# Optimization experiments

Measured on AMD Instinct MI355X. Metric: run time of the kernel, lower is better.

## Reference

```python
import jax, jax.numpy as jnp
import numpy as np

B, T, HID = 16, 512, 1024
NH, NKV, D = 8, 4, 128
THETA = 10000.0


def setup_inputs() -> dict:
    key = jax.random.key(0)
    k0, k1, k2, k3, k4 = jax.random.split(key, 5)
    s = 0.02
    return {
        "hidden_states": jax.random.normal(k0, (B, T, HID), dtype=jnp.float32),
        "Wq": s * jax.random.normal(k1, (HID, NH * D), dtype=jnp.float32),
        "Wk": s * jax.random.normal(k2, (HID, NKV * D), dtype=jnp.float32),
        "Wv": s * jax.random.normal(k3, (HID, NKV * D), dtype=jnp.float32),
        "Wo": s * jax.random.normal(k4, (NH * D, HID), dtype=jnp.float32),
    }


def _rotate_half(x):
    x1, x2 = x[..., : x.shape[-1] // 2], x[..., x.shape[-1] // 2:]
    return jnp.concatenate((-x2, x1), axis=-1)


def reference(hidden_states, Wq, Wk, Wv, Wo):
    b, t, _ = hidden_states.shape
    # projections -> [B, H, T, D]
    q = (hidden_states @ Wq).reshape(b, t, NH, D).transpose(0, 2, 1, 3)
    k = (hidden_states @ Wk).reshape(b, t, NKV, D).transpose(0, 2, 1, 3)
    v = (hidden_states @ Wv).reshape(b, t, NKV, D).transpose(0, 2, 1, 3)

    # RoPE: cos/sin [T, D]
    inv_freq = 1.0 / (THETA ** (jnp.arange(0, D, 2, dtype=jnp.float32) / D))
    freqs = jnp.outer(jnp.arange(t, dtype=jnp.float32), inv_freq)
    emb = jnp.concatenate((freqs, freqs), axis=-1)
    cos, sin = jnp.cos(emb), jnp.sin(emb)
    q = q * cos + _rotate_half(q) * sin
    k = k * cos + _rotate_half(k) * sin

    # repeat_interleave KV heads to match query heads (GQA)
    groups = NH // NKV
    k = jnp.repeat(k, groups, axis=1)  # [B, NH, T, D]
    v = jnp.repeat(v, groups, axis=1)

    scale = 1.0 / jnp.sqrt(jnp.float32(D))
    attn = jnp.einsum("bhtd,bhsd->bhts", q, k) * scale  # [B, NH, T, T]
    causal = jnp.triu(jnp.ones((t, t), dtype=bool), k=1)
    attn = jnp.where(causal, -jnp.inf, attn)
    attn = jax.nn.softmax(attn, axis=-1)  # dropout p=0 (eval)

    out = jnp.einsum("bhts,bhsd->bhtd", attn, v)
    out = out.transpose(0, 2, 1, 3).reshape(b, t, NH * D)
    return out @ Wo  # [B, T, HID]
```

## Files before the change

### kernel.cpp

```cpp
#include <hip/hip_runtime.h>
#include <hip/hip_bf16.h>
#include <math.h>

#define Bn 16
#define Tn 512
#define HIDn 1024
#define NHn 8
#define NKVn 4
#define Dn 128

typedef __attribute__((ext_vector_type(8))) short short8;
typedef __attribute__((ext_vector_type(4))) float floatx4;

__device__ __forceinline__ short bf16r(float f) {
  __hip_bfloat16 h = __float2bfloat16(f);
  return *(short*)&h;
}
__device__ __forceinline__ float bf16f(short s) {
  __hip_bfloat16 h = *(__hip_bfloat16*)&s;
  return __bfloat162float(h);
}

__device__ __forceinline__ void g2l16(const short* g, short* l) {
  __builtin_amdgcn_global_load_lds(
      (const __attribute__((address_space(1))) void*)g,
      (__attribute__((address_space(3))) void*)l, 16, 0, 0);
}

__global__ __launch_bounds__(256) void prep_kernel(const float* __restrict__ X,
                                                   const float* __restrict__ Wq,
                                                   const float* __restrict__ Wk,
                                                   const float* __restrict__ Wv,
                                                   const float* __restrict__ Wo,
                                                   short* __restrict__ Xb,
                                                   short* __restrict__ BtQKV,
                                                   short* __restrict__ Wot) {
  __shared__ float tile[32][33];
  int bid = blockIdx.x;
  if (bid < 4096) {
    int i = bid * 256 + threadIdx.x;
    const float4* p = reinterpret_cast<const float4*>(X) + (size_t)i * 2;
    float4 a = p[0], b = p[1];
    short8 o;
    o[0] = bf16r(a.x); o[1] = bf16r(a.y); o[2] = bf16r(a.z); o[3] = bf16r(a.w);
    o[4] = bf16r(b.x); o[5] = bf16r(b.y); o[6] = bf16r(b.z); o[7] = bf16r(b.w);
    reinterpret_cast<short8*>(Xb)[i] = o;
    return;
  }
  int t = bid - 4096;
  const float* in;
  short* out;
  int N;
  if (t < 1024)      { in = Wq; out = BtQKV;               N = 1024; }
  else if (t < 1536) { t -= 1024; in = Wk; out = BtQKV + 1024 * 1024; N = 512; }
  else if (t < 2048) { t -= 1536; in = Wv; out = BtQKV + 1536 * 1024; N = 512; }
  else               { t -= 2048; in = Wo; out = Wot;                N = 1024; }
  int ntx = N >> 5;
  int n0 = (t % ntx) * 32, k0 = (t / ntx) * 32;
  int tx = threadIdx.x & 31, ty = threadIdx.x >> 5;
  for (int i = 0; i < 32; i += 8)
    tile[ty + i][tx] = in[(size_t)(k0 + ty + i) * N + n0 + tx];
  __syncthreads();
  for (int i = 0; i < 32; i += 8)
    out[(size_t)(n0 + ty + i) * 1024 + k0 + tx] = bf16r(tile[tx][ty + i]);
}

__global__ __launch_bounds__(512, 2) void gemm_qkv(const short* __restrict__ A,
                                                   const short* __restrict__ Bt,
                                                   short* __restrict__ Cqkv,
                                                   short* __restrict__ Vt) {
  __shared__ __align__(16) short SH[65536];
  const int tid = threadIdx.x;
  const int wave = tid >> 6, lane = tid & 63;
  const int quad = lane >> 4, l16 = lane & 15;
  const int wr = wave >> 2, wc = wave & 3;
  int fid = blockIdx.y * 8 + blockIdx.x;
  int swz = (fid & 7) * 32 + (fid >> 3);
  const int bx = swz & 7;
  const int m0 = (swz >> 3) << 8, n0 = bx << 8;
  const int nt = 16;

  floatx4 acc[2][2][4][2];
#pragma unroll
  for (int r = 0; r < 2; ++r)
#pragma unroll
    for (int c = 0; c < 2; ++c)
#pragma unroll
      for (int mi = 0; mi < 4; ++mi)
#pragma unroll
        for (int ni = 0; ni < 2; ++ni)
          acc[r][c][mi][ni] = (floatx4){0.f, 0.f, 0.f, 0.f};

  const int srow = tid >> 3;
  const int schunk = (tid & 7) ^ (srow & 7);

#define STAGE(tile_, src_, row0_, ldso_)                                             \
  do {                                                                               \
    int t_ = (tile_);                                                                \
    if (t_ < nt) {                                                                   \
      short* bb_ = SH + ((t_ & 1) << 15) + (ldso_);                                  \
      const short* sp_ =                                                             \
          (src_) + ((size_t)((row0_) + srow) << 10) + (t_ << 6) + (schunk << 3);     \
      g2l16(sp_, bb_ + (wave << 9));                                                 \
      g2l16(sp_ + (64 << 10), bb_ + 4096 + (wave << 9));                             \
    }                                                                                \
  } while (0)

#define LDA(dst_, rhalf_)                                                            \
  do {                                                                               \
    _Pragma("unroll") for (int mi = 0; mi < 4; ++mi) {                               \
      int R = (rhalf_) * 128 + wr * 64 + mi * 16 + l16;                              \
      _Pragma("unroll") for (int k = 0; k < 2; ++k) {                                \
        int pos = (k * 4 + quad) ^ (R & 7);                                          \
        dst_[mi][k] = *(const short8*)&Ab[R * 64 + pos * 8];                         \
      }                                                                              \
    }                                                                                \
  } while (0)

#define LDB(dst_, chalf_)                                                            \
  do {                                                                               \
    _Pragma("unroll") for (int ni = 0; ni < 2; ++ni) {                               \
      int R = (chalf_) * 128 + wc * 32 + ni * 16 + l16;                              \
      _Pragma("unroll") for (int k = 0; k < 2; ++k) {                                \
        int pos = (k * 4 + quad) ^ (R & 7);                                          \
        dst_[ni][k] = *(const short8*)&Bb[R * 64 + pos * 8];                         \
      }                                                                              \
    }                                                                                \
  } while (0)

#define MFMA_Q(r_, c_, a_, b_)                                                       \
  do {                                                                               \
    _Pragma("unroll") for (int mi = 0; mi < 4; ++mi)                                 \
        _Pragma("unroll") for (int ni = 0; ni < 2; ++ni) {                           \
      acc[r_][c_][mi][ni] = __builtin_amdgcn_mfma_f32_16x16x32_bf16(                 \
          a_[mi][0], b_[ni][0], acc[r_][c_][mi][ni], 0, 0, 0);                       \
      acc[r_][c_][mi][ni] = __builtin_amdgcn_mfma_f32_16x16x32_bf16(                 \
          a_[mi][1], b_[ni][1], acc[r_][c_][mi][ni], 0, 0, 0);                       \
    }                                                                                \
  } while (0)

#define PH_OPEN()                                                                    \
  do {                                                                               \
    __builtin_amdgcn_s_barrier();                                                    \
    __builtin_amdgcn_s_setprio(1);                                                   \
  } while (0)
#define PH_CLOSE()                                                                   \
  do {                                                                               \
    __builtin_amdgcn_s_setprio(0);                                                   \
    __builtin_amdgcn_s_barrier();                                                    \
  } while (0)

  STAGE(0, A, m0, 0);
  STAGE(0, Bt, n0 + 128, 24576);
  STAGE(0, Bt, n0, 16384);
  STAGE(0, A, m0 + 128, 8192);
  STAGE(1, A, m0, 0);
  STAGE(1, Bt, n0 + 128, 24576);
  STAGE(1, Bt, n0, 16384);
  asm volatile("s_waitcnt vmcnt(6)" ::: "memory");
  __builtin_amdgcn_s_barrier();

  short8 afA[4][2], afB[4][2], bf0[2][2], bf1[2][2];
  for (int g = 0; g < nt; ++g) {
    const short* Ab = SH + ((g & 1) << 15);
    const short* Bb = Ab + 16384;
    LDA(afA, 0);
    LDB(bf0, 0);
    LDB(bf1, 1);
    STAGE(g + 1, A, m0 + 128, 8192);
    PH_OPEN();
    MFMA_Q(0, 0, afA, bf0);
    PH_CLOSE();
    LDA(afB, 1);
    STAGE(g + 2, A, m0, 0);
    PH_OPEN();
    MFMA_Q(0, 1, afA, bf1);
    PH_CLOSE();
    STAGE(g + 2, Bt, n0 + 128, 24576);
    PH_OPEN();
    MFMA_Q(1, 1, afB, bf1);
    PH_CLOSE();
    STAGE(g + 2, Bt, n0, 16384);
    PH_OPEN();
    MFMA_Q(1, 0, afB, bf0);
    __builtin_amdgcn_s_setprio(0);
    if (g + 2 < nt)
      asm volatile("s_waitcnt vmcnt(6)" ::: "memory");
    else
      asm volatile("s_waitcnt vmcnt(0)" ::: "memory");
    __builtin_amdgcn_s_barrier();
  }

  if (bx < 6) {
#pragma unroll
    for (int r = 0; r < 2; ++r)
#pragma unroll
      for (int c = 0; c < 2; ++c)
#pragma unroll
        for (int mi = 0; mi < 4; ++mi)
#pragma unroll
          for (int ni = 0; ni < 2; ++ni)
#pragma unroll
            for (int rr = 0; rr < 4; ++rr) {
              int row = m0 + r * 128 + wr * 64 + mi * 16 + quad * 4 + rr;
              int col = n0 + c * 128 + wc * 32 + ni * 16 + l16;
              Cqkv[(size_t)row * 2048 + col] = bf16r(acc[r][c][mi][ni][rr]);
            }
  } else {
    const int b = m0 >> 9, t0 = m0 & (Tn - 1);
#pragma unroll
    for (int ch = 0; ch < 2; ++ch) {
      __syncthreads();
#pragma unroll
      for (int r = 0; r < 2; ++r)
#pragma unroll
        for (int mi = 0; mi < 4; ++mi)
#pragma unroll
          for (int ni = 0; ni < 2; ++ni)
#pragma unroll
            for (int rr = 0; rr < 4; ++rr) {
              int t = r * 128 + wr * 64 + mi * 16 + quad * 4 + rr;
              int d = wc * 32 + ni * 16 + l16;
              SH[d * 264 + t] = bf16r(acc[r][ch][mi][ni][rr]);
            }
      __syncthreads();
      int kv = (bx - 6) * 2 + ch;
#pragma unroll
      for (int u = 0; u < 8; ++u) {
        int idx = tid + u * 512;
        int d = idx >> 5, tb = (idx & 31) << 3;
        short8 vv = *(short8*)&SH[d * 264 + tb];
        *(short8*)&Vt[((size_t)(b * NKVn + kv) * 128 + d) * Tn + t0 + tb] = vv;
      }
    }
  }
#undef STAGE
#undef LDA
#undef LDB
#undef MFMA_Q
#undef PH_OPEN
#undef PH_CLOSE
}

__global__ void rope_k_kernel(short* __restrict__ C) {
  int idx = blockIdx.x * blockDim.x + threadIdx.x;
  int vec = idx & 7;
  int head = (idx >> 3) & 3;
  int bt = idx >> 5;
  int t = bt & (Tn - 1);
  int i0 = vec * 8;
  size_t base = (size_t)bt * 2048 + 1024 + head * 128 + i0;
  short8 x1 = *(short8*)&C[base];
  short8 x2 = *(short8*)&C[base + 64];
  short8 o1, o2;
  float tf = (float)t;
#pragma unroll
  for (int j = 0; j < 8; ++j) {
    float a = tf * exp2f(-0.2076205059f * (float)(i0 + j));
    float s, c;
    __sincosf(a, &s, &c);
    float v1 = bf16f(x1[j]), v2 = bf16f(x2[j]);
    o1[j] = bf16r(v1 * c - v2 * s);
    o2[j] = bf16r(v2 * c + v1 * s);
  }
  *(short8*)&C[base] = o1;
  *(short8*)&C[base + 64] = o2;
}

__global__ __launch_bounds__(512, 2) void gemm_out(const short* __restrict__ A,
                                                   const short* __restrict__ Bt,
                                                   float* __restrict__ Cout) {
  __shared__ __align__(16) short SH[49152];
  const int tid = threadIdx.x;
  const int wave = tid >> 6, lane = tid & 63;
  const int quad = lane >> 4, l16 = lane & 15;
  const int wr = wave >> 2, wc = wave & 3;
  int fid = blockIdx.y * 8 + blockIdx.x;
  int swz = (fid & 7) * 32 + (fid >> 3);
  const int m0 = (swz >> 3) << 8;
  const int n0 = (swz & 7) << 7;
  const int nt = 16;

  floatx4 acc[2][4][2];
#pragma unroll
  for (int r = 0; r < 2; ++r)
#pragma unroll
    for (int mi = 0; mi < 4; ++mi)
#pragma unroll
      for (int ni = 0; ni < 2; ++ni)
        acc[r][mi][ni] = (floatx4){0.f, 0.f, 0.f, 0.f};

  const int srow = tid >> 3;
  const int schunk = (tid & 7) ^ (srow & 7);

#define STAGE(tile_, src_, row0_, ldso_)                                             \
  do {                                                                               \
    int t_ = (tile_);                                                                \
    if (t_ < nt) {                                                                   \
      short* bb_ = SH + (t_ & 1) * 24576 + (ldso_);                                  \
      const short* sp_ =                                                             \
          (src_) + ((size_t)((row0_) + srow) << 10) + (t_ << 6) + (schunk << 3);     \
      g2l16(sp_, bb_ + (wave << 9));                                                 \
      g2l16(sp_ + (64 << 10), bb_ + 4096 + (wave << 9));                             \
    }                                                                                \
  } while (0)

#define LDA(dst_, rhalf_)                                                            \
  do {                                                                               \
    _Pragma("unroll") for (int mi = 0; mi < 4; ++mi) {                               \
      int R = (rhalf_) * 128 + wr * 64 + mi * 16 + l16;                              \
      _Pragma("unroll") for (int k = 0; k < 2; ++k) {                                \
        int pos = (k * 4 + quad) ^ (R & 7);                                          \
        dst_[mi][k] = *(const short8*)&Ab[R * 64 + pos * 8];                         \
      }                                                                              \
    }                                                                                \
  } while (0)

#define LDB()                                                                        \
  do {                                                                               \
    _Pragma("unroll") for (int ni = 0; ni < 2; ++ni) {                               \
      int R = wc * 32 + ni * 16 + l16;                                               \
      _Pragma("unroll") for (int k = 0; k < 2; ++k) {                                \
        int pos = (k * 4 + quad) ^ (R & 7);                                          \
        bf0[ni][k] = *(const short8*)&Bb[R * 64 + pos * 8];                          \
      }                                                                              \
    }                                                                                \
  } while (0)

#define MFMA_Q(r_, a_)                                                               \
  do {                                                                               \
    _Pragma("unroll") for (int mi = 0; mi < 4; ++mi)                                 \
        _Pragma("unroll") for (int ni = 0; ni < 2; ++ni) {                           \
      acc[r_][mi][ni] = __builtin_amdgcn_mfma_f32_16x16x32_bf16(                     \
          a_[mi][0], bf0[ni][0], acc[r_][mi][ni], 0, 0, 0);                          \
      acc[r_][mi][ni] = __builtin_amdgcn_mfma_f32_16x16x32_bf16(                     \
          a_[mi][1], bf0[ni][1], acc[r_][mi][ni], 0, 0, 0);                          \
    }                                                                                \
  } while (0)

#define PH_OPEN()                                                                    \
  do {                                                                               \
    __builtin_amdgcn_s_barrier();                                                    \
    __builtin_amdgcn_s_setprio(1);                                                   \
  } while (0)
#define PH_CLOSE()                                                                   \
  do {                                                                               \
    __builtin_amdgcn_s_setprio(0);                                                   \
    __builtin_amdgcn_s_barrier();                                                    \
  } while (0)

  STAGE(0, A, m0, 0);
  STAGE(0, Bt, n0, 16384);
  STAGE(0, A, m0 + 128, 8192);
  STAGE(1, A, m0, 0);
  STAGE(1, Bt, n0, 16384);
  asm volatile("s_waitcnt vmcnt(4)" ::: "memory");
  __builtin_amdgcn_s_barrier();

  short8 afA[4][2], afB[4][2], bf0[2][2];
  for (int g = 0; g < nt; ++g) {
    const short* Ab = SH + (g & 1) * 24576;
    const short* Bb = Ab + 16384;
    LDA(afA, 0);
    LDB();
    LDA(afB, 1);
    STAGE(g + 1, A, m0 + 128, 8192);
    PH_OPEN();
    MFMA_Q(0, afA);
    PH_CLOSE();
    STAGE(g + 2, A, m0, 0);
    STAGE(g + 2, Bt, n0, 16384);
    PH_OPEN();
    MFMA_Q(1, afB);
    __builtin_amdgcn_s_setprio(0);
    if (g + 2 < nt)
      asm volatile("s_waitcnt vmcnt(4)" ::: "memory");
    else
      asm volatile("s_waitcnt vmcnt(0)" ::: "memory");
    __builtin_amdgcn_s_barrier();
  }

#pragma unroll
  for (int r = 0; r < 2; ++r)
#pragma unroll
    for (int mi = 0; mi < 4; ++mi)
#pragma unroll
      for (int ni = 0; ni < 2; ++ni)
#pragma unroll
        for (int rr = 0; rr < 4; ++rr) {
          int row = m0 + r * 128 + wr * 64 + mi * 16 + quad * 4 + rr;
          int col = n0 + wc * 32 + ni * 16 + l16;
          Cout[(size_t)row * 1024 + col] = acc[r][mi][ni][rr];
        }
#undef STAGE
#undef LDA
#undef LDB
#undef MFMA_Q
#undef PH_OPEN
#undef PH_CLOSE
}

__global__ __launch_bounds__(256) void attn_kernel(const short* __restrict__ Cqkv,
                                                   const short* __restrict__ Vt,
                                                   short* __restrict__ Aout) {
  __shared__ __align__(16) short SH[20992];
  short* Ks = SH;
  short (*Ps)[16][72] = reinterpret_cast<short(*)[16][72]>(SH + 16384);
  const int tid = threadIdx.x;
  const int wave = tid >> 6, lane = tid & 63;
  const int quad = lane >> 4, l16 = lane & 15;
  const int blk = blockIdx.x;
  const int qt = 7 - (blk >> 7);
  const int h = blk & 7, b = (blk >> 3) & 15;
  const int kvh = h >> 1;
  const short* Qp = Cqkv + (size_t)b * Tn * 2048 + h * 128;
  const short* Kp = Cqkv + (size_t)b * Tn * 2048 + 1024 + kvh * 128;
  const short* Vtp = Vt + (size_t)(b * NKVn + kvh) * 128 * Tn;

  const int qrow0 = qt * 64 + wave * 16;
  const float scale = 0.12753378904f;

#define STAGEK(k0_, b_)                                                       \
  do {                                                                        \
    _Pragma("unroll") for (int v = 0; v < 4; ++v) {                           \
      int s_ = tid + v * 256;                                                 \
      int r_ = s_ >> 4, c_ = (s_ & 15) ^ (r_ & 15);                           \
      g2l16(&Kp[(size_t)((k0_) + r_) * 2048 + c_ * 8],                        \
            Ks + ((b_) << 13) + (v * 256 + wave * 64) * 8);                   \
    }                                                                         \
  } while (0)

  short8 qf[4];
#pragma unroll
  for (int kc = 0; kc < 4; ++kc)
    qf[kc] = *(const short8*)&Qp[(size_t)(qrow0 + l16) * 2048 + kc * 32 + quad * 8];

  STAGEK(0, 0);

  {
    float tf = (float)(qrow0 + l16);
#pragma unroll
    for (int kc = 0; kc < 2; ++kc)
#pragma unroll
      for (int j = 0; j < 8; ++j) {
        int d = kc * 32 + quad * 8 + j;
        float a = tf * exp2f(-0.2076205059f * (float)d);
        float s, c;
        __sincosf(a, &s, &c);
        float x1 = bf16f(qf[kc][j]), x2 = bf16f(qf[kc + 2][j]);
        qf[kc][j] = bf16r((x1 * c - x2 * s) * scale);
        qf[kc + 2][j] = bf16r((x2 * c + x1 * s) * scale);
      }
  }

  floatx4 o[8];
  float l_part[4];
#pragma unroll
  for (int ni = 0; ni < 8; ++ni) o[ni] = (floatx4){0.f, 0.f, 0.f, 0.f};
#pragma unroll
  for (int r = 0; r < 4; ++r) l_part[r] = 0.f;

  const int ntiles = qt + 1;
  __syncthreads();

  for (int it = 0; it < ntiles; ++it) {
    const int k0 = it << 6;
    const short* Kb = Ks + ((it & 1) << 13);

    short8 vf0[8], vf1[8];
#pragma unroll
    for (int ni = 0; ni < 8; ++ni) {
      const short* vp = &Vtp[(size_t)(ni * 16 + l16) * Tn + k0 + quad * 8];
      vf0[ni] = *(const short8*)vp;
      vf1[ni] = *(const short8*)(vp + 32);
    }

    if (it + 1 < ntiles) STAGEK(k0 + 64, (it + 1) & 1);

    floatx4 s[4];
    __builtin_amdgcn_s_setprio(1);
#pragma unroll
    for (int ni = 0; ni < 4; ++ni) {
      s[ni] = (floatx4){0.f, 0.f, 0.f, 0.f};
      short8 kf[4];
#pragma unroll
      for (int kc = 0; kc < 4; ++kc) {
        int R = ni * 16 + l16;
        int pos = (kc * 4 + quad) ^ (R & 15);
        kf[kc] = *(short8*)&Kb[R * 128 + pos * 8];
      }
#pragma unroll
      for (int kc = 0; kc < 4; ++kc)
        s[ni] = __builtin_amdgcn_mfma_f32_16x16x32_bf16(qf[kc], kf[kc], s[ni], 0, 0, 0);
    }
    __builtin_amdgcn_s_setprio(0);

    const bool diag = (k0 + 63 > qrow0);
#pragma unroll
    for (int ni = 0; ni < 4; ++ni)
#pragma unroll
      for (int r = 0; r < 4; ++r) {
        float p = exp2f(s[ni][r]);
        if (diag) {
          int key = k0 + ni * 16 + l16;
          int qr = qrow0 + quad * 4 + r;
          if (key > qr) p = 0.f;
        }
        s[ni][r] = p;
        l_part[r] += p;
      }

#pragma unroll
    for (int ni = 0; ni < 4; ++ni)
#pragma unroll
      for (int r = 0; r < 4; ++r)
        Ps[wave][quad * 4 + r][ni * 16 + l16] = bf16r(s[ni][r]);

    short8 pf[2];
#pragma unroll
    for (int kc = 0; kc < 2; ++kc)
      pf[kc] = *(short8*)&Ps[wave][l16][kc * 32 + quad * 8];
    __builtin_amdgcn_s_setprio(1);
#pragma unroll
    for (int ni = 0; ni < 8; ++ni) {
      o[ni] = __builtin_amdgcn_mfma_f32_16x16x32_bf16(pf[0], vf0[ni], o[ni], 0, 0, 0);
      o[ni] = __builtin_amdgcn_mfma_f32_16x16x32_bf16(pf[1], vf1[ni], o[ni], 0, 0, 0);
    }
    __builtin_amdgcn_s_setprio(0);

    if (it + 1 < ntiles) __syncthreads();
  }
#undef STAGEK

  float inv[4];
#pragma unroll
  for (int r = 0; r < 4; ++r) {
    float rs = l_part[r];
#pragma unroll
    for (int off = 8; off >= 1; off >>= 1) rs += __shfl_xor(rs, off, 16);
    inv[r] = 1.0f / rs;
  }
#pragma unroll
  for (int ni = 0; ni < 8; ++ni)
#pragma unroll
    for (int r = 0; r < 4; ++r) {
      int t = qrow0 + quad * 4 + r;
      int d = ni * 16 + l16;
      Aout[((size_t)b * Tn + t) * 1024 + h * 128 + d] = bf16r(o[ni][r] * inv[r]);
    }
}

extern "C" void kernel_launch(void* const* d_in, const int* in_sizes, int n_in,
                              void* d_out, int out_size, void* d_ws, size_t ws_size,
                              hipStream_t stream) {
  const float* X  = (const float*)d_in[0];
  const float* Wq = (const float*)d_in[1];
  const float* Wk = (const float*)d_in[2];
  const float* Wv = (const float*)d_in[3];
  const float* Wo = (const float*)d_in[4];

  char* ws = (char*)d_ws;
  short* Xb    = (short*)(ws);
  short* BtQKV = (short*)(ws + (16ull << 20));
  short* Wot   = (short*)(ws + (20ull << 20));
  short* Cqkv  = (short*)(ws + (22ull << 20));
  short* Vt    = (short*)(ws + (54ull << 20));
  short* Aout  = (short*)(ws + (62ull << 20));

  prep_kernel<<<7168, 256, 0, stream>>>(X, Wq, Wk, Wv, Wo, Xb, BtQKV, Wot);
  gemm_qkv<<<dim3(8, 32), 512, 0, stream>>>(Xb, BtQKV, Cqkv, Vt);
  rope_k_kernel<<<1024, 256, 0, stream>>>(Cqkv);
  attn_kernel<<<1024, 256, 0, stream>>>(Cqkv, Vt, Aout);
  gemm_out<<<dim3(8, 32), 512, 0, stream>>>(Aout, Wot, (float*)d_out);
}
```

Before: 196.1 us.

## Process both GQA query heads per attention block to share K/V loads

Each attention block now handles both query heads that share one KV head, so K tiles staged in LDS and V fragments loaded from global memory are reused for two heads. The grid halves from 1024 to 512 blocks, and each wave keeps two sets of Q fragments, score and output accumulators, with a doubled P buffer in LDS. This cuts K/V traffic and staging per unit of work, at the cost of higher register and LDS use per block, which can lower occupancy, and fewer blocks to spread across CUs.

```diff
diff --git a/kernel.cpp b/kernel.cpp
--- a/kernel.cpp
+++ b/kernel.cpp
@@ -403,17 +403,16 @@
 __global__ __launch_bounds__(256) void attn_kernel(const short* __restrict__ Cqkv,
                                                    const short* __restrict__ Vt,
                                                    short* __restrict__ Aout) {
-  __shared__ __align__(16) short SH[20992];
+  __shared__ __align__(16) short SH[25600];
   short* Ks = SH;
-  short (*Ps)[16][72] = reinterpret_cast<short(*)[16][72]>(SH + 16384);
+  short (*Ps)[2][16][72] = reinterpret_cast<short(*)[2][16][72]>(SH + 16384);
   const int tid = threadIdx.x;
   const int wave = tid >> 6, lane = tid & 63;
   const int quad = lane >> 4, l16 = lane & 15;
   const int blk = blockIdx.x;
-  const int qt = 7 - (blk >> 7);
-  const int h = blk & 7, b = (blk >> 3) & 15;
-  const int kvh = h >> 1;
-  const short* Qp = Cqkv + (size_t)b * Tn * 2048 + h * 128;
+  const int qt = 7 - (blk >> 6);
+  const int kvh = blk & 3, b = (blk >> 2) & 15;
+  const short* Qp = Cqkv + (size_t)b * Tn * 2048 + (kvh * 2) * 128;
   const short* Kp = Cqkv + (size_t)b * Tn * 2048 + 1024 + kvh * 128;
   const short* Vtp = Vt + (size_t)(b * NKVn + kvh) * 128 * Tn;
 
@@ -430,10 +429,13 @@
     }                                                                         \
   } while (0)
 
-  short8 qf[4];
-#pragma unroll
-  for (int kc = 0; kc < 4; ++kc)
-    qf[kc] = *(const short8*)&Qp[(size_t)(qrow0 + l16) * 2048 + kc * 32 + quad * 8];
+  short8 qf0[4], qf1[4];
+#pragma unroll
+  for (int kc = 0; kc < 4; ++kc) {
+    const short* qp = &Qp[(size_t)(qrow0 + l16) * 2048 + kc * 32 + quad * 8];
+    qf0[kc] = *(const short8*)qp;
+    qf1[kc] = *(const short8*)(qp + 128);
+  }
 
   STAGEK(0, 0);
 
@@ -447,18 +449,24 @@
         float a = tf * exp2f(-0.2076205059f * (float)d);
         float s, c;
         __sincosf(a, &s, &c);
-        float x1 = bf16f(qf[kc][j]), x2 = bf16f(qf[kc + 2][j]);
-        qf[kc][j] = bf16r((x1 * c - x2 * s) * scale);
-        qf[kc + 2][j] = bf16r((x2 * c + x1 * s) * scale);
+        float x1 = bf16f(qf0[kc][j]), x2 = bf16f(qf0[kc + 2][j]);
+        qf0[kc][j] = bf16r((x1 * c - x2 * s) * scale);
+        qf0[kc + 2][j] = bf16r((x2 * c + x1 * s) * scale);
+        float y1 = bf16f(qf1[kc][j]), y2 = bf16f(qf1[kc + 2][j]);
+        qf1[kc][j] = bf16r((y1 * c - y2 * s) * scale);
+        qf1[kc + 2][j] = bf16r((y2 * c + y1 * s) * scale);
       }
   }
 
-  floatx4 o[8];
-  float l_part[4];
-#pragma unroll
-  for (int ni = 0; ni < 8; ++ni) o[ni] = (floatx4){0.f, 0.f, 0.f, 0.f};
-#pragma unroll
-  for (int r = 0; r < 4; ++r) l_part[r] = 0.f;
+  floatx4 o0[8], o1[8];
+  float l0[4], l1[4];
+#pragma unroll
+  for (int ni = 0; ni < 8; ++ni) {
+    o0[ni] = (floatx4){0.f, 0.f, 0.f, 0.f};
+    o1[ni] = (floatx4){0.f, 0.f, 0.f, 0.f};
+  }
+#pragma unroll
+  for (int r = 0; r < 4; ++r) { l0[r] = 0.f; l1[r] = 0.f; }
 
   const int ntiles = qt + 1;
   __syncthreads();
@@ -477,11 +485,12 @@
 
     if (it + 1 < ntiles) STAGEK(k0 + 64, (it + 1) & 1);
 
-    floatx4 s[4];
+    floatx4 s0[4], s1[4];
     __builtin_amdgcn_s_setprio(1);
 #pragma unroll
     for (int ni = 0; ni < 4; ++ni) {
-      s[ni] = (floatx4){0.f, 0.f, 0.f, 0.f};
+      s0[ni] = (floatx4){0.f, 0.f, 0.f, 0.f};
+      s1[ni] = (floatx4){0.f, 0.f, 0.f, 0.f};
       short8 kf[4];
 #pragma unroll
       for (int kc = 0; kc < 4; ++kc) {
@@ -490,8 +499,10 @@
         kf[kc] = *(short8*)&Kb[R * 128 + pos * 8];
       }
 #pragma unroll
-      for (int kc = 0; kc < 4; ++kc)
-        s[ni] = __builtin_amdgcn_mfma_f32_16x16x32_bf16(qf[kc], kf[kc], s[ni], 0, 0, 0);
+      for (int kc = 0; kc < 4; ++kc) {
+        s0[ni] = __builtin_amdgcn_mfma_f32_16x16x32_bf16(qf0[kc], kf[kc], s0[ni], 0, 0, 0);
+        s1[ni] = __builtin_amdgcn_mfma_f32_16x16x32_bf16(qf1[kc], kf[kc], s1[ni], 0, 0, 0);
+      }
     }
     __builtin_amdgcn_s_setprio(0);
 
@@ -500,31 +511,32 @@
     for (int ni = 0; ni < 4; ++ni)
 #pragma unroll
       for (int r = 0; r < 4; ++r) {
-        float p = exp2f(s[ni][r]);
+        float p0 = exp2f(s0[ni][r]);
+        float p1 = exp2f(s1[ni][r]);
         if (diag) {
           int key = k0 + ni * 16 + l16;
           int qr = qrow0 + quad * 4 + r;
-          if (key > qr) p = 0.f;
+          if (key > qr) { p0 = 0.f; p1 = 0.f; }
         }
-        s[ni][r] = p;
-        l_part[r] += p;
+        l0[r] += p0;
+        l1[r] += p1;
+        Ps[wave][0][quad * 4 + r][ni * 16 + l16] = bf16r(p0);
+        Ps[wave][1][quad * 4 + r][ni * 16 + l16] = bf16r(p1);
       }
 
-#pragma unroll
-    for (int ni = 0; ni < 4; ++ni)
-#pragma unroll
-      for (int r = 0; r < 4; ++r)
-        Ps[wave][quad * 4 + r][ni * 16 + l16] = bf16r(s[ni][r]);
-
-    short8 pf[2];
-#pragma unroll
-    for (int kc = 0; kc < 2; ++kc)
-      pf[kc] = *(short8*)&Ps[wave][l16][kc * 32 + quad * 8];
+    short8 pf0[2], pf1[2];
+#pragma unroll
+    for (int kc = 0; kc < 2; ++kc) {
+      pf0[kc] = *(short8*)&Ps[wave][0][l16][kc * 32 + quad * 8];
+      pf1[kc] = *(short8*)&Ps[wave][1][l16][kc * 32 + quad * 8];
+    }
     __builtin_amdgcn_s_setprio(1);
 #pragma unroll
     for (int ni = 0; ni < 8; ++ni) {
-      o[ni] = __builtin_amdgcn_mfma_f32_16x16x32_bf16(pf[0], vf0[ni], o[ni], 0, 0, 0);
-      o[ni] = __builtin_amdgcn_mfma_f32_16x16x32_bf16(pf[1], vf1[ni], o[ni], 0, 0, 0);
+      o0[ni] = __builtin_amdgcn_mfma_f32_16x16x32_bf16(pf0[0], vf0[ni], o0[ni], 0, 0, 0);
+      o0[ni] = __builtin_amdgcn_mfma_f32_16x16x32_bf16(pf0[1], vf1[ni], o0[ni], 0, 0, 0);
+      o1[ni] = __builtin_amdgcn_mfma_f32_16x16x32_bf16(pf1[0], vf0[ni], o1[ni], 0, 0, 0);
+      o1[ni] = __builtin_amdgcn_mfma_f32_16x16x32_bf16(pf1[1], vf1[ni], o1[ni], 0, 0, 0);
     }
     __builtin_amdgcn_s_setprio(0);
 
@@ -532,21 +544,28 @@
   }
 #undef STAGEK
 
-  float inv[4];
+  float inv0[4], inv1[4];
 #pragma unroll
   for (int r = 0; r < 4; ++r) {
-    float rs = l_part[r];
-#pragma unroll
-    for (int off = 8; off >= 1; off >>= 1) rs += __shfl_xor(rs, off, 16);
-    inv[r] = 1.0f / rs;
-  }
+    float r0 = l0[r], r1 = l1[r];
+#pragma unroll
+    for (int off = 8; off >= 1; off >>= 1) {
+      r0 += __shfl_xor(r0, off, 16);
+      r1 += __shfl_xor(r1, off, 16);
+    }
+    inv0[r] = 1.0f / r0;
+    inv1[r] = 1.0f / r1;
+  }
+  const int h0 = kvh * 2;
 #pragma unroll
   for (int ni = 0; ni < 8; ++ni)
 #pragma unroll
     for (int r = 0; r < 4; ++r) {
       int t = qrow0 + quad * 4 + r;
       int d = ni * 16 + l16;
-      Aout[((size_t)b * Tn + t) * 1024 + h * 128 + d] = bf16r(o[ni][r] * inv[r]);
+      size_t base = ((size_t)b * Tn + t) * 1024 + h0 * 128 + d;
+      Aout[base] = bf16r(o0[ni][r] * inv0[r]);
+      Aout[base + 128] = bf16r(o1[ni][r] * inv1[r]);
     }
 }
 
@@ -570,6 +589,6 @@
   prep_kernel<<<7168, 256, 0, stream>>>(X, Wq, Wk, Wv, Wo, Xb, BtQKV, Wot);
   gemm_qkv<<<dim3(8, 32), 512, 0, stream>>>(Xb, BtQKV, Cqkv, Vt);
   rope_k_kernel<<<1024, 256, 0, stream>>>(Cqkv);
-  attn_kernel<<<1024, 256, 0, stream>>>(Cqkv, Vt, Aout);
+  attn_kernel<<<512, 256, 0, stream>>>(Cqkv, Vt, Aout);
   gemm_out<<<dim3(8, 32), 512, 0, stream>>>(Aout, Wot, (float*)d_out);
 }
```

Result: faster. 187.1 us (-4.6%).
